# Kernel tuning notes

Measured on AMD Instinct MI355X. Metric: run time of the kernel, lower is better.

The kernel has to match this reference:

```python
import jax, jax.numpy as jnp
import numpy as np

IN_DIM = 128
OUT_DIM = 128
H = 8
HD = OUT_DIM // H  # 16
EPS = 1e-5
NEG = -1e30


def setup_inputs() -> dict:
    key = jax.random.key(0)
    ks = jax.random.split(key, 10)
    B, N = 8, 1024
    h = jax.random.normal(ks[0], (B, N, IN_DIM), dtype=jnp.float32)
    adj_mask = jax.random.randint(ks[1], (B, N, N), 0, 2, dtype=jnp.int32)
    s = 1.0 / np.sqrt(IN_DIM)
    W = jax.random.normal(ks[2], (H, IN_DIM, HD), dtype=jnp.float32) * s
    a = jax.random.normal(ks[3], (H, 2 * HD), dtype=jnp.float32) * (1.0 / np.sqrt(2 * HD))
    ln1_g = jnp.ones((OUT_DIM,), jnp.float32)
    ln1_b = jnp.zeros((OUT_DIM,), jnp.float32)
    w1 = jax.random.normal(ks[4], (OUT_DIM, 2 * OUT_DIM), dtype=jnp.float32) * (1.0 / np.sqrt(OUT_DIM))
    b1 = jnp.zeros((2 * OUT_DIM,), jnp.float32)
    w2 = jax.random.normal(ks[5], (2 * OUT_DIM, OUT_DIM), dtype=jnp.float32) * (1.0 / np.sqrt(2 * OUT_DIM))
    b2 = jnp.zeros((OUT_DIM,), jnp.float32)
    ln2_g = jnp.ones((OUT_DIM,), jnp.float32)
    ln2_b = jnp.zeros((OUT_DIM,), jnp.float32)
    return dict(h=h, adj_mask=adj_mask, W=W, a=a, ln1_g=ln1_g, ln1_b=ln1_b,
                w1=w1, b1=b1, w2=w2, b2=b2, ln2_g=ln2_g, ln2_b=ln2_b)


def _layernorm(x, g, b):
    mu = jnp.mean(x, axis=-1, keepdims=True)
    var = jnp.mean(jnp.square(x - mu), axis=-1, keepdims=True)
    return (x - mu) * jax.lax.rsqrt(var + EPS) * g + b


def reference(h, adj_mask, W, a, ln1_g, ln1_b, w1, b1, w2, b2, ln2_g, ln2_b):
    B, N, _ = h.shape
    # Per-head projection: (B,H,N,HD)
    Wh = jnp.einsum('bni,hid->bhnd', h, W)
    # a.[Wh_i, Wh_j] = a_src.Wh_i + a_dst.Wh_j (decompose concat-score)
    a_src, a_dst = a[:, :HD], a[:, HD:]
    s_i = jnp.einsum('bhnd,hd->bhn', Wh, a_src)  # source term
    s_j = jnp.einsum('bhnd,hd->bhn', Wh, a_dst)  # target term
    e = s_i[:, :, :, None] + s_j[:, :, None, :]  # (B,H,N,N)
    e = jnp.where(e >= 0, e, 0.2 * e)            # LeakyReLU(0.2)
    mask = (adj_mask != 0)[:, None, :, :]        # (B,1,N,N)
    e = jnp.where(mask, e, NEG)
    alpha = jax.nn.softmax(e, axis=-1)
    # rows with no neighbors -> NaN in torch softmax -> zeroed; replicate
    row_valid = jnp.any(mask, axis=-1, keepdims=True)  # (B,1,N,1)
    alpha = jnp.where(row_valid, alpha, 0.0)
    # dropout in eval mode = identity
    h_heads = jnp.einsum('bhnm,bhmd->bhnd', alpha, Wh)
    h_cat = h_heads.transpose(0, 2, 1, 3).reshape(B, N, H * HD)
    # residual (in_dim == out_dim here)
    h_cat = _layernorm(h_cat + h, ln1_g, ln1_b)
    ffn = jnp.maximum(h_cat @ w1 + b1, 0.0) @ w2 + b2
    return _layernorm(h_cat + ffn, ln2_g, ln2_b)
```

## Files before the change

kernel.cpp:

```cpp
#include <hip/hip_runtime.h>
#include <hip/hip_bf16.h>

#define IN_DIM 128
#define OUT_DIM 128
#define NHEAD 8
#define HD 16
#define BB 8
#define NN 1024
#define LOG2E 1.44269504f

typedef unsigned long long u64;
typedef float f32x4 __attribute__((ext_vector_type(4)));
typedef short bf16x8 __attribute__((ext_vector_type(8)));


__global__ __launch_bounds__(256) void k_prep(
    const float* __restrict__ hin, const float* __restrict__ W,
    const float* __restrict__ a, const int* __restrict__ adj,
    unsigned* __restrict__ bits_t, unsigned short* __restrict__ whT,
    float* __restrict__ si_g, float* __restrict__ sj_g,
    const float* __restrict__ w1, const float* __restrict__ w2,
    unsigned short* __restrict__ w1T, unsigned short* __restrict__ w2T)
{
    __shared__ float smem[32 * 132];
    int blk = blockIdx.x;
    int t = threadIdx.x;

    if (blk < 256) {
        int b = blk >> 5, ntile = blk & 31;
        const float* hrow = hin + ((size_t)b * NN + ntile * 32) * IN_DIM;
#pragma unroll
        for (int it = 0; it < 4; ++it) {
            int g = t + 256 * it;
            int row = g >> 5, c4 = g & 31;
            float4 v = ((const float4*)hrow)[g];
            *(float4*)&smem[row * 132 + c4 * 4] = v;
        }
        __syncthreads();

        int d4 = t & 3;
        int hq = (t >> 2) & 7;
        int ngrp = t >> 5;
        float acc[4][4];
#pragma unroll
        for (int q = 0; q < 4; ++q)
#pragma unroll
            for (int dd = 0; dd < 4; ++dd) acc[q][dd] = 0.f;

        for (int i4 = 0; i4 < 32; ++i4) {
            float4 wf[4];
#pragma unroll
            for (int k = 0; k < 4; ++k)
                wf[k] = *(const float4*)&W[((size_t)hq * 128 + i4 * 4 + k) * 16 + d4 * 4];
            float4 hv[4];
#pragma unroll
            for (int q = 0; q < 4; ++q)
                hv[q] = *(const float4*)&smem[(ngrp * 4 + q) * 132 + i4 * 4];
#pragma unroll
            for (int q = 0; q < 4; ++q) {
                acc[q][0] += hv[q].x * wf[0].x + hv[q].y * wf[1].x + hv[q].z * wf[2].x + hv[q].w * wf[3].x;
                acc[q][1] += hv[q].x * wf[0].y + hv[q].y * wf[1].y + hv[q].z * wf[2].y + hv[q].w * wf[3].y;
                acc[q][2] += hv[q].x * wf[0].z + hv[q].y * wf[1].z + hv[q].z * wf[2].z + hv[q].w * wf[3].z;
                acc[q][3] += hv[q].x * wf[0].w + hv[q].y * wf[1].w + hv[q].z * wf[2].w + hv[q].w * wf[3].w;
            }
        }

        int bh = b * NHEAD + hq;
        int rowbase = ntile * 32 + ngrp * 4;
        int p0 = ((rowbase >> 8) << 8) | ((rowbase >> 2) & 63);

        float asrc[4], adst[4];
#pragma unroll
        for (int dd = 0; dd < 4; ++dd) {
            asrc[dd] = a[hq * 32 + d4 * 4 + dd];
            adst[dd] = a[hq * 32 + 16 + d4 * 4 + dd];
        }
#pragma unroll
        for (int q = 0; q < 4; ++q) {
            float psi = acc[q][0] * asrc[0] + acc[q][1] * asrc[1] + acc[q][2] * asrc[2] + acc[q][3] * asrc[3];
            float psj = acc[q][0] * adst[0] + acc[q][1] * adst[1] + acc[q][2] * adst[2] + acc[q][3] * adst[3];
            psi += __shfl_xor(psi, 1); psi += __shfl_xor(psi, 2);
            psj += __shfl_xor(psj, 1); psj += __shfl_xor(psj, 2);
            if (d4 == 0) {
                si_g[(size_t)bh * NN + rowbase + q] = psi * LOG2E;
                sj_g[(size_t)bh * NN + p0 + q * 64] = psj * LOG2E;
            }
        }

#pragma unroll
        for (int dd = 0; dd < 4; ++dd) {
            unsigned u0, u1;
            asm("v_cvt_pk_bf16_f32 %0, %1, %2" : "=v"(u0) : "v"(acc[0][dd]), "v"(acc[1][dd]));
            asm("v_cvt_pk_bf16_f32 %0, %1, %2" : "=v"(u1) : "v"(acc[2][dd]), "v"(acc[3][dd]));
            size_t basei = (size_t)(bh * 16 + d4 * 4 + dd) * 1024 + p0;
            whT[basei]       = (unsigned short)(u0 & 0xffff);
            whT[basei + 64]  = (unsigned short)(u0 >> 16);
            whT[basei + 128] = (unsigned short)(u1 & 0xffff);
            whT[basei + 192] = (unsigned short)(u1 >> 16);
        }
    } else if (blk < 2304) {
        int lane = t & 63;
        int wave_id = (blk - 256) * 4 + (t >> 6);
        int b = wave_id >> 10, i = wave_id & 1023;
        const int4* rowp = (const int4*)(adj + ((size_t)(b * 1024 + i)) * 1024);
        int4 v0 = rowp[lane];
        int4 v1 = rowp[64 + lane];
        int4 v2 = rowp[128 + lane];
        int4 v3 = rowp[192 + lane];
        u64 B0x = __ballot(v0.x != 0), B0y = __ballot(v0.y != 0), B0z = __ballot(v0.z != 0), B0w = __ballot(v0.w != 0);
        u64 B1x = __ballot(v1.x != 0), B1y = __ballot(v1.y != 0), B1z = __ballot(v1.z != 0), B1w = __ballot(v1.w != 0);
        u64 B2x = __ballot(v2.x != 0), B2y = __ballot(v2.y != 0), B2z = __ballot(v2.z != 0), B2w = __ballot(v2.w != 0);
        u64 B3x = __ballot(v3.x != 0), B3y = __ballot(v3.y != 0), B3z = __ballot(v3.z != 0), B3w = __ballot(v3.w != 0);
        if (lane == 0) {
            unsigned* dst = bits_t + (size_t)b * 32 * 1024 + i;
#define STW(ch, c, B) \
            dst[((ch) * 8 + (c) * 2 + 0) * 1024] = (unsigned)(B); \
            dst[((ch) * 8 + (c) * 2 + 1) * 1024] = (unsigned)((B) >> 32);
            STW(0, 0, B0x) STW(0, 1, B0y) STW(0, 2, B0z) STW(0, 3, B0w)
            STW(1, 0, B1x) STW(1, 1, B1y) STW(1, 2, B1z) STW(1, 3, B1w)
            STW(2, 0, B2x) STW(2, 1, B2y) STW(2, 2, B2z) STW(2, 3, B2w)
            STW(3, 0, B3x) STW(3, 1, B3y) STW(3, 2, B3z) STW(3, 3, B3w)
#undef STW
        }
    } else {
        int bb = blk - 2304;
        const float* src; unsigned short* dst; int R, C;
        if (bb < 32) { src = w1; dst = w1T; R = 128; C = 256; }
        else         { src = w2; dst = w2T; R = 256; C = 128; bb -= 32; }
        int tpr = C >> 5;
        int tr = bb / tpr, tc = bb - tr * tpr;
        int r0 = tr << 5, c0 = tc << 5;
        int lr = t >> 5, lc = t & 31;
#pragma unroll
        for (int p = 0; p < 4; ++p)
            smem[(lr + p * 8) * 33 + lc] = src[(size_t)(r0 + lr + p * 8) * C + c0 + lc];
        __syncthreads();
#pragma unroll
        for (int p = 0; p < 4; ++p) {
            __hip_bfloat16 bv = __float2bfloat16(smem[lc * 33 + lr + p * 8]);
            dst[(size_t)(c0 + lr + p * 8) * R + r0 + lc] = *(unsigned short*)&bv;
        }
    }
}

__global__ __launch_bounds__(512, 3) void k_attn(
    const unsigned short* __restrict__ whT,
    const unsigned* __restrict__ bits_t,
    const float* __restrict__ si_g, const float* __restrict__ sj_g,
    float* __restrict__ hh)
{
    __shared__ __align__(16) unsigned short whT_s[16 * 1032];
    __shared__ __align__(16) float ejp_s[NN];
    __shared__ __align__(16) float ejn_s[NN];
    int t = threadIdx.x;
    int blk = blockIdx.x;
    int part = blk & 7;
    int bh = blk >> 3;
    int hq = bh & 7, b = bh >> 3;
    int blkrow = part * 128;

    {
        const uint4* src = (const uint4*)(whT + (size_t)bh * 16 * 1024);
#pragma unroll
        for (int it = 0; it < 4; ++it) {
            int g = t + 512 * it;
            int d = g >> 7, c8 = g & 127;
            uint4 v = src[g];
            *(uint4*)&whT_s[d * 1032 + c8 * 8] = v;
        }
#pragma unroll
        for (int jt = 0; jt < 2; ++jt) {
            int j = t + jt * 512;
            float sjv = sj_g[(size_t)bh * NN + j];
            float ep, en;
            asm("v_exp_f32 %0, %1" : "=v"(ep) : "v"(sjv));
            asm("v_exp_f32 %0, %1" : "=v"(en) : "v"(0.2f * sjv));
            ejp_s[j] = ep;
            ejn_s[j] = en;
        }
    }
    __syncthreads();

    int wv = t >> 6, lane = t & 63;
    int lo16 = lane & 15, g = lane >> 4;
    int row = blkrow + wv * 16 + lo16;
    float siL = si_g[(size_t)bh * NN + row];
    float esip, esin;
    asm("v_exp_f32 %0, %1" : "=v"(esip) : "v"(siL));
    asm("v_exp_f32 %0, %1" : "=v"(esin) : "v"(0.2f * siL));
    const unsigned* mcol = bits_t + (size_t)b * 32 * 1024 + row;

    f32x4 acc = {0.f, 0.f, 0.f, 0.f};
    float lsA = 0.f, lsB = 0.f;
    unsigned m = mcol[0];
#pragma unroll 4
    for (int kt = 0; kt < 32; ++kt) {
        unsigned m_next = (kt < 31) ? mcol[(size_t)(kt + 1) * 1024] : 0u;
        bf16x8 bfrag = *(const bf16x8*)&whT_s[lo16 * 1032 + kt * 32 + g * 8];
        float4 pa = *(const float4*)&ejp_s[kt * 32 + g * 8];
        float4 pb = *(const float4*)&ejp_s[kt * 32 + g * 8 + 4];
        float4 na = *(const float4*)&ejn_s[kt * 32 + g * 8];
        float4 nb = *(const float4*)&ejn_s[kt * 32 + g * 8 + 4];
        unsigned mm = m >> (g * 8);
        float ep[8] = {pa.x, pa.y, pa.z, pa.w, pb.x, pb.y, pb.z, pb.w};
        float en[8] = {na.x, na.y, na.z, na.w, nb.x, nb.y, nb.z, nb.w};
        union { bf16x8 v; unsigned u[4]; } af;
#pragma unroll
        for (int e2 = 0; e2 < 4; ++e2) {
            float q0 = fmaxf(esip * ep[2 * e2], esin * en[2 * e2]);
            float q1 = fmaxf(esip * ep[2 * e2 + 1], esin * en[2 * e2 + 1]);
            q0 = ((mm >> (2 * e2)) & 1) ? q0 : 0.f;
            q1 = ((mm >> (2 * e2 + 1)) & 1) ? q1 : 0.f;
            lsA += q0;
            lsB += q1;
            asm("v_cvt_pk_bf16_f32 %0, %1, %2" : "=v"(af.u[e2]) : "v"(q0), "v"(q1));
        }
        acc = __builtin_amdgcn_mfma_f32_16x16x32_bf16(af.v, bfrag, acc, 0, 0, 0);
        m = m_next;
    }

    float lsum = lsA + lsB;
    lsum += __shfl_xor(lsum, 16);
    lsum += __shfl_xor(lsum, 32);

    float* obase = hh + ((size_t)b * NN + blkrow + wv * 16) * OUT_DIM + hq * HD + lo16;
#pragma unroll
    for (int q = 0; q < 4; ++q) {
        float ls = __shfl(lsum, 4 * g + q);
        float r = (ls > 0.f) ? 1.0f / ls : 0.f;
        obase[(size_t)(4 * g + q) * OUT_DIM] = acc[q] * r;
    }
}

__global__ __launch_bounds__(512, 1) void k_ffn(const float* __restrict__ hhs,
                                                const float* __restrict__ hin,
                                                const float* __restrict__ g1,
                                                const float* __restrict__ bt1,
                                                const unsigned short* __restrict__ w1T,
                                                const float* __restrict__ bb1,
                                                const unsigned short* __restrict__ w2T,
                                                const float* __restrict__ bb2,
                                                const float* __restrict__ g2,
                                                const float* __restrict__ bt2,
                                                float* __restrict__ out) {
    __shared__ float xc_f[32][128];
    __shared__ float y_f[32][132];
    __shared__ __align__(16) unsigned short xc_bf[32 * 128];
    __shared__ __align__(16) unsigned short hid_bf[32 * 256];

    int t = threadIdx.x;
    int R0 = blockIdx.x * 32;
    int wv = t >> 6, lane = t & 63;
    int lo = lane & 15, g = lane >> 4;

    bf16x8 b1f[2][4];
#pragma unroll
    for (int jt = 0; jt < 2; ++jt) {
        int n = (wv * 2 + jt) * 16 + lo;
#pragma unroll
        for (int kt = 0; kt < 4; ++kt)
            b1f[jt][kt] = *(const bf16x8*)&w1T[(size_t)n * 128 + kt * 32 + g * 8];
    }
    bf16x8 b2f[8];
    {
        int n = wv * 16 + lo;
#pragma unroll
        for (int kt = 0; kt < 8; ++kt)
            b2f[kt] = *(const bf16x8*)&w2T[(size_t)n * 256 + kt * 32 + g * 8];
    }
    float b1v[2];
    b1v[0] = bb1[(wv * 2 + 0) * 16 + lo];
    b1v[1] = bb1[(wv * 2 + 1) * 16 + lo];
    float b2v = bb2[wv * 16 + lo];

    {
        int r = t >> 4, c = t & 15;
        size_t row = (size_t)(R0 + r) * 128;
        float4 ha = *(const float4*)&hhs[row + c * 8];
        float4 hb = *(const float4*)&hhs[row + c * 8 + 4];
        float4 ia = *(const float4*)&hin[row + c * 8];
        float4 ib = *(const float4*)&hin[row + c * 8 + 4];
        float x[8] = {ha.x + ia.x, ha.y + ia.y, ha.z + ia.z, ha.w + ia.w,
                      hb.x + ib.x, hb.y + ib.y, hb.z + ib.z, hb.w + ib.w};
        float s = 0.f, s2 = 0.f;
#pragma unroll
        for (int j = 0; j < 8; ++j) { s += x[j]; s2 += x[j] * x[j]; }
#pragma unroll
        for (int off = 8; off > 0; off >>= 1) {
            s += __shfl_xor(s, off);
            s2 += __shfl_xor(s2, off);
        }
        float mu = s * (1.f / 128.f);
        float var = s2 * (1.f / 128.f) - mu * mu;
        float rs = rsqrtf(var + 1e-5f);
        float4 ga = *(const float4*)&g1[c * 8], gb = *(const float4*)&g1[c * 8 + 4];
        float4 ba = *(const float4*)&bt1[c * 8], bb = *(const float4*)&bt1[c * 8 + 4];
        float gg[8] = {ga.x, ga.y, ga.z, ga.w, gb.x, gb.y, gb.z, gb.w};
        float bbv[8] = {ba.x, ba.y, ba.z, ba.w, bb.x, bb.y, bb.z, bb.w};
        float xo[8];
#pragma unroll
        for (int j = 0; j < 8; ++j) xo[j] = (x[j] - mu) * rs * gg[j] + bbv[j];
        *(float4*)&xc_f[r][c * 8]     = make_float4(xo[0], xo[1], xo[2], xo[3]);
        *(float4*)&xc_f[r][c * 8 + 4] = make_float4(xo[4], xo[5], xo[6], xo[7]);
        union { uint4 v; unsigned u[4]; } pk;
#pragma unroll
        for (int q = 0; q < 4; ++q)
            asm("v_cvt_pk_bf16_f32 %0, %1, %2" : "=v"(pk.u[q]) : "v"(xo[2 * q]), "v"(xo[2 * q + 1]));
        int byte = (r * 256 + c * 16) ^ ((r & 7) << 4);
        *(uint4*)((char*)xc_bf + byte) = pk.v;
    }
    __syncthreads();

    {
        bf16x8 af[2][4];
#pragma unroll
        for (int mt = 0; mt < 2; ++mt) {
            int m = mt * 16 + lo;
#pragma unroll
            for (int kt = 0; kt < 4; ++kt) {
                int byte = (m * 256 + kt * 64 + g * 16) ^ ((m & 7) << 4);
                af[mt][kt] = *(const bf16x8*)((const char*)xc_bf + byte);
            }
        }
#pragma unroll
        for (int mt = 0; mt < 2; ++mt)
#pragma unroll
            for (int jt = 0; jt < 2; ++jt) {
                f32x4 acc = {0.f, 0.f, 0.f, 0.f};
#pragma unroll
                for (int kt = 0; kt < 4; ++kt)
                    acc = __builtin_amdgcn_mfma_f32_16x16x32_bf16(af[mt][kt], b1f[jt][kt], acc, 0, 0, 0);
                int n = (wv * 2 + jt) * 16 + lo;
#pragma unroll
                for (int q = 0; q < 4; ++q) {
                    float hv = fmaxf(acc[q] + b1v[jt], 0.f);
                    int m = mt * 16 + 4 * g + q;
                    int byte = (m * 512 + n * 2) ^ ((m & 7) << 4);
                    __hip_bfloat16 bv = __float2bfloat16(hv);
                    *(unsigned short*)((char*)hid_bf + byte) = *(unsigned short*)&bv;
                }
            }
    }
    __syncthreads();

    {
        f32x4 acc2[2] = {{0.f, 0.f, 0.f, 0.f}, {0.f, 0.f, 0.f, 0.f}};
#pragma unroll
        for (int mt = 0; mt < 2; ++mt) {
            int m = mt * 16 + lo;
#pragma unroll
            for (int kt = 0; kt < 8; ++kt) {
                int byte = (m * 512 + kt * 64 + g * 16) ^ ((m & 7) << 4);
                bf16x8 a = *(const bf16x8*)((const char*)hid_bf + byte);
                acc2[mt] = __builtin_amdgcn_mfma_f32_16x16x32_bf16(a, b2f[kt], acc2[mt], 0, 0, 0);
            }
        }
        int n = wv * 16 + lo;
#pragma unroll
        for (int mt = 0; mt < 2; ++mt)
#pragma unroll
            for (int q = 0; q < 4; ++q)
                y_f[mt * 16 + 4 * g + q][n] = acc2[mt][q] + b2v;
    }
    __syncthreads();

    {
        int r = t >> 4, c = t & 15;
        float xv[8];
        float s = 0.f, s2 = 0.f;
#pragma unroll
        for (int j = 0; j < 8; ++j) {
            float v = xc_f[r][c * 8 + j] + y_f[r][c * 8 + j];
            xv[j] = v; s += v; s2 += v * v;
        }
#pragma unroll
        for (int off = 8; off > 0; off >>= 1) {
            s += __shfl_xor(s, off);
            s2 += __shfl_xor(s2, off);
        }
        float mu = s * (1.f / 128.f);
        float var = s2 * (1.f / 128.f) - mu * mu;
        float rs = rsqrtf(var + 1e-5f);
        float4 ga = *(const float4*)&g2[c * 8], gb = *(const float4*)&g2[c * 8 + 4];
        float4 ba = *(const float4*)&bt2[c * 8], bb = *(const float4*)&bt2[c * 8 + 4];
        float o[8] = {(xv[0] - mu) * rs * ga.x + ba.x, (xv[1] - mu) * rs * ga.y + ba.y,
                      (xv[2] - mu) * rs * ga.z + ba.z, (xv[3] - mu) * rs * ga.w + ba.w,
                      (xv[4] - mu) * rs * gb.x + bb.x, (xv[5] - mu) * rs * gb.y + bb.y,
                      (xv[6] - mu) * rs * gb.z + bb.z, (xv[7] - mu) * rs * gb.w + bb.w};
        size_t row = (size_t)(R0 + r) * 128;
        *(float4*)&out[row + c * 8]     = make_float4(o[0], o[1], o[2], o[3]);
        *(float4*)&out[row + c * 8 + 4] = make_float4(o[4], o[5], o[6], o[7]);
    }
}

extern "C" void kernel_launch(void* const* d_in, const int* in_sizes, int n_in,
                              void* d_out, int out_size, void* d_ws, size_t ws_size,
                              hipStream_t stream) {
    const float* hin  = (const float*)d_in[0];
    const int*   adj  = (const int*)d_in[1];
    const float* W    = (const float*)d_in[2];
    const float* a    = (const float*)d_in[3];
    const float* ln1g = (const float*)d_in[4];
    const float* ln1b = (const float*)d_in[5];
    const float* w1   = (const float*)d_in[6];
    const float* b1   = (const float*)d_in[7];
    const float* w2   = (const float*)d_in[8];
    const float* b2   = (const float*)d_in[9];
    const float* ln2g = (const float*)d_in[10];
    const float* ln2b = (const float*)d_in[11];
    float* out = (float*)d_out;

    unsigned* bits_t    = (unsigned*)d_ws;
    unsigned short* whT = (unsigned short*)((char*)d_ws + (1u << 20));
    float* si_g         = (float*)((char*)d_ws + (3u << 20));
    float* sj_g         = (float*)((char*)d_ws + (3u << 20) + (256u << 10));
    float* hh           = (float*)((char*)d_ws + (3u << 20) + (512u << 10));
    unsigned short* w1T = (unsigned short*)((char*)d_ws + (7u << 20) + (512u << 10));
    unsigned short* w2T = (unsigned short*)((char*)d_ws + (7u << 20) + (512u << 10) + 65536);

    k_prep<<<2368, 256, 0, stream>>>(hin, W, a, adj, bits_t, whT, si_g, sj_g,
                                     w1, w2, w1T, w2T);
    k_attn<<<BB * NHEAD * 8, 512, 0, stream>>>(whT, bits_t, si_g, sj_g, hh);
    k_ffn<<<BB * NN / 32, 512, 0, stream>>>(hh, hin, ln1g, ln1b, w1T, b1, w2T, b2, ln2g, ln2b, out);
}
```

Measured before the change: 64.20 us.

## Split prep kernel into separate launches and stage transposed W in LDS

```diff
diff --git a/kernel.cpp b/kernel.cpp
--- a/kernel.cpp
+++ b/kernel.cpp
@@ -14,132 +14,149 @@
 typedef short bf16x8 __attribute__((ext_vector_type(8)));
 
 
-__global__ __launch_bounds__(256) void k_prep(
+__global__ __launch_bounds__(256) void k_wh(
     const float* __restrict__ hin, const float* __restrict__ W,
-    const float* __restrict__ a, const int* __restrict__ adj,
-    unsigned* __restrict__ bits_t, unsigned short* __restrict__ whT,
-    float* __restrict__ si_g, float* __restrict__ sj_g,
-    const float* __restrict__ w1, const float* __restrict__ w2,
-    unsigned short* __restrict__ w1T, unsigned short* __restrict__ w2T)
+    const float* __restrict__ a,
+    unsigned short* __restrict__ whT, float* __restrict__ si_g,
+    float* __restrict__ sj_g)
 {
-    __shared__ float smem[32 * 132];
+    extern __shared__ float smem[];
+    float* h_s  = smem;
+    float* wt_s = smem + 32 * 132;
+    int t = threadIdx.x;
     int blk = blockIdx.x;
+    int b = blk >> 5;
+    int ntile = blk & 31;
+    const float* hrow = hin + ((size_t)b * NN + ntile * 32) * IN_DIM;
+
+#pragma unroll
+    for (int it = 0; it < 4; ++it) {
+        int g = t + 256 * it;
+        int row = g >> 5, c4 = g & 31;
+        float4 v = ((const float4*)hrow)[g];
+        *(float4*)&h_s[row * 132 + c4 * 4] = v;
+    }
+    for (int g = t; g < (NHEAD * IN_DIM * HD) / 4; g += 256) {
+        int hh = g >> 9;
+        int rem = g & 511;
+        int i = rem >> 2, d4 = rem & 3;
+        float4 v = ((const float4*)W)[g];
+        wt_s[(hh * 16 + d4 * 4 + 0) * 132 + i] = v.x;
+        wt_s[(hh * 16 + d4 * 4 + 1) * 132 + i] = v.y;
+        wt_s[(hh * 16 + d4 * 4 + 2) * 132 + i] = v.z;
+        wt_s[(hh * 16 + d4 * 4 + 3) * 132 + i] = v.w;
+    }
+    __syncthreads();
+
+    int d4 = t & 3;
+    int hq = (t >> 2) & 7;
+    int ngrp = t >> 5;
+    float acc[4][4];
+#pragma unroll
+    for (int q = 0; q < 4; ++q)
+#pragma unroll
+        for (int dd = 0; dd < 4; ++dd) acc[q][dd] = 0.f;
+
+    for (int i4 = 0; i4 < 32; ++i4) {
+        float4 wr[4], hv[4];
+#pragma unroll
+        for (int dd = 0; dd < 4; ++dd)
+            wr[dd] = *(const float4*)&wt_s[(hq * 16 + d4 * 4 + dd) * 132 + i4 * 4];
+#pragma unroll
+        for (int q = 0; q < 4; ++q)
+            hv[q] = *(const float4*)&h_s[(ngrp * 4 + q) * 132 + i4 * 4];
+#pragma unroll
+        for (int q = 0; q < 4; ++q)
+#pragma unroll
+            for (int dd = 0; dd < 4; ++dd)
+                acc[q][dd] += hv[q].x * wr[dd].x + hv[q].y * wr[dd].y +
+                              hv[q].z * wr[dd].z + hv[q].w * wr[dd].w;
+    }
+
+    int bh = b * NHEAD + hq;
+    int rowbase = ntile * 32 + ngrp * 4;
+    int p0 = ((rowbase >> 8) << 8) | ((rowbase >> 2) & 63);
+
+    float asrc[4], adst[4];
+#pragma unroll
+    for (int dd = 0; dd < 4; ++dd) {
+        asrc[dd] = a[hq * 32 + d4 * 4 + dd];
+        adst[dd] = a[hq * 32 + 16 + d4 * 4 + dd];
+    }
+#pragma unroll
+    for (int q = 0; q < 4; ++q) {
+        float psi = acc[q][0] * asrc[0] + acc[q][1] * asrc[1] + acc[q][2] * asrc[2] + acc[q][3] * asrc[3];
+        float psj = acc[q][0] * adst[0] + acc[q][1] * adst[1] + acc[q][2] * adst[2] + acc[q][3] * adst[3];
+        psi += __shfl_xor(psi, 1); psi += __shfl_xor(psi, 2);
+        psj += __shfl_xor(psj, 1); psj += __shfl_xor(psj, 2);
+        if (d4 == 0) {
+            si_g[(size_t)bh * NN + rowbase + q] = psi * LOG2E;
+            sj_g[(size_t)bh * NN + p0 + q * 64] = psj * LOG2E;
+        }
+    }
+
+#pragma unroll
+    for (int dd = 0; dd < 4; ++dd) {
+        unsigned u0, u1;
+        asm("v_cvt_pk_bf16_f32 %0, %1, %2" : "=v"(u0) : "v"(acc[0][dd]), "v"(acc[1][dd]));
+        asm("v_cvt_pk_bf16_f32 %0, %1, %2" : "=v"(u1) : "v"(acc[2][dd]), "v"(acc[3][dd]));
+        size_t basei = (size_t)(bh * 16 + d4 * 4 + dd) * 1024 + p0;
+        whT[basei]       = (unsigned short)(u0 & 0xffff);
+        whT[basei + 64]  = (unsigned short)(u0 >> 16);
+        whT[basei + 128] = (unsigned short)(u1 & 0xffff);
+        whT[basei + 192] = (unsigned short)(u1 >> 16);
+    }
+}
+
+__global__ __launch_bounds__(256) void k_pack(const int* __restrict__ adj,
+                                              unsigned* __restrict__ bits_t) {
     int t = threadIdx.x;
-
-    if (blk < 256) {
-        int b = blk >> 5, ntile = blk & 31;
-        const float* hrow = hin + ((size_t)b * NN + ntile * 32) * IN_DIM;
-#pragma unroll
-        for (int it = 0; it < 4; ++it) {
-            int g = t + 256 * it;
-            int row = g >> 5, c4 = g & 31;
-            float4 v = ((const float4*)hrow)[g];
-            *(float4*)&smem[row * 132 + c4 * 4] = v;
-        }
-        __syncthreads();
-
-        int d4 = t & 3;
-        int hq = (t >> 2) & 7;
-        int ngrp = t >> 5;
-        float acc[4][4];
-#pragma unroll
-        for (int q = 0; q < 4; ++q)
-#pragma unroll
-            for (int dd = 0; dd < 4; ++dd) acc[q][dd] = 0.f;
-
-        for (int i4 = 0; i4 < 32; ++i4) {
-            float4 wf[4];
-#pragma unroll
-            for (int k = 0; k < 4; ++k)
-                wf[k] = *(const float4*)&W[((size_t)hq * 128 + i4 * 4 + k) * 16 + d4 * 4];
-            float4 hv[4];
-#pragma unroll
-            for (int q = 0; q < 4; ++q)
-                hv[q] = *(const float4*)&smem[(ngrp * 4 + q) * 132 + i4 * 4];
-#pragma unroll
-            for (int q = 0; q < 4; ++q) {
-                acc[q][0] += hv[q].x * wf[0].x + hv[q].y * wf[1].x + hv[q].z * wf[2].x + hv[q].w * wf[3].x;
-                acc[q][1] += hv[q].x * wf[0].y + hv[q].y * wf[1].y + hv[q].z * wf[2].y + hv[q].w * wf[3].y;
-                acc[q][2] += hv[q].x * wf[0].z + hv[q].y * wf[1].z + hv[q].z * wf[2].z + hv[q].w * wf[3].z;
-                acc[q][3] += hv[q].x * wf[0].w + hv[q].y * wf[1].w + hv[q].z * wf[2].w + hv[q].w * wf[3].w;
-            }
-        }
-
-        int bh = b * NHEAD + hq;
-        int rowbase = ntile * 32 + ngrp * 4;
-        int p0 = ((rowbase >> 8) << 8) | ((rowbase >> 2) & 63);
-
-        float asrc[4], adst[4];
-#pragma unroll
-        for (int dd = 0; dd < 4; ++dd) {
-            asrc[dd] = a[hq * 32 + d4 * 4 + dd];
-            adst[dd] = a[hq * 32 + 16 + d4 * 4 + dd];
-        }
-#pragma unroll
-        for (int q = 0; q < 4; ++q) {
-            float psi = acc[q][0] * asrc[0] + acc[q][1] * asrc[1] + acc[q][2] * asrc[2] + acc[q][3] * asrc[3];
-            float psj = acc[q][0] * adst[0] + acc[q][1] * adst[1] + acc[q][2] * adst[2] + acc[q][3] * adst[3];
-            psi += __shfl_xor(psi, 1); psi += __shfl_xor(psi, 2);
-            psj += __shfl_xor(psj, 1); psj += __shfl_xor(psj, 2);
-            if (d4 == 0) {
-                si_g[(size_t)bh * NN + rowbase + q] = psi * LOG2E;
-                sj_g[(size_t)bh * NN + p0 + q * 64] = psj * LOG2E;
-            }
-        }
-
-#pragma unroll
-        for (int dd = 0; dd < 4; ++dd) {
-            unsigned u0, u1;
-            asm("v_cvt_pk_bf16_f32 %0, %1, %2" : "=v"(u0) : "v"(acc[0][dd]), "v"(acc[1][dd]));
-            asm("v_cvt_pk_bf16_f32 %0, %1, %2" : "=v"(u1) : "v"(acc[2][dd]), "v"(acc[3][dd]));
-            size_t basei = (size_t)(bh * 16 + d4 * 4 + dd) * 1024 + p0;
-            whT[basei]       = (unsigned short)(u0 & 0xffff);
-            whT[basei + 64]  = (unsigned short)(u0 >> 16);
-            whT[basei + 128] = (unsigned short)(u1 & 0xffff);
-            whT[basei + 192] = (unsigned short)(u1 >> 16);
-        }
-    } else if (blk < 2304) {
-        int lane = t & 63;
-        int wave_id = (blk - 256) * 4 + (t >> 6);
-        int b = wave_id >> 10, i = wave_id & 1023;
-        const int4* rowp = (const int4*)(adj + ((size_t)(b * 1024 + i)) * 1024);
-        int4 v0 = rowp[lane];
-        int4 v1 = rowp[64 + lane];
-        int4 v2 = rowp[128 + lane];
-        int4 v3 = rowp[192 + lane];
-        u64 B0x = __ballot(v0.x != 0), B0y = __ballot(v0.y != 0), B0z = __ballot(v0.z != 0), B0w = __ballot(v0.w != 0);
-        u64 B1x = __ballot(v1.x != 0), B1y = __ballot(v1.y != 0), B1z = __ballot(v1.z != 0), B1w = __ballot(v1.w != 0);
-        u64 B2x = __ballot(v2.x != 0), B2y = __ballot(v2.y != 0), B2z = __ballot(v2.z != 0), B2w = __ballot(v2.w != 0);
-        u64 B3x = __ballot(v3.x != 0), B3y = __ballot(v3.y != 0), B3z = __ballot(v3.z != 0), B3w = __ballot(v3.w != 0);
-        if (lane == 0) {
-            unsigned* dst = bits_t + (size_t)b * 32 * 1024 + i;
+    int lane = t & 63;
+    int wave_id = blockIdx.x * 4 + (t >> 6);
+    int b = wave_id >> 10, i = wave_id & 1023;
+    const int4* rowp = (const int4*)(adj + ((size_t)(b * 1024 + i)) * 1024);
+    int4 v0 = rowp[lane];
+    int4 v1 = rowp[64 + lane];
+    int4 v2 = rowp[128 + lane];
+    int4 v3 = rowp[192 + lane];
+    u64 B0x = __ballot(v0.x != 0), B0y = __ballot(v0.y != 0), B0z = __ballot(v0.z != 0), B0w = __ballot(v0.w != 0);
+    u64 B1x = __ballot(v1.x != 0), B1y = __ballot(v1.y != 0), B1z = __ballot(v1.z != 0), B1w = __ballot(v1.w != 0);
+    u64 B2x = __ballot(v2.x != 0), B2y = __ballot(v2.y != 0), B2z = __ballot(v2.z != 0), B2w = __ballot(v2.w != 0);
+    u64 B3x = __ballot(v3.x != 0), B3y = __ballot(v3.y != 0), B3z = __ballot(v3.z != 0), B3w = __ballot(v3.w != 0);
+    if (lane == 0) {
+        unsigned* dst = bits_t + (size_t)b * 32 * 1024 + i;
 #define STW(ch, c, B) \
-            dst[((ch) * 8 + (c) * 2 + 0) * 1024] = (unsigned)(B); \
-            dst[((ch) * 8 + (c) * 2 + 1) * 1024] = (unsigned)((B) >> 32);
-            STW(0, 0, B0x) STW(0, 1, B0y) STW(0, 2, B0z) STW(0, 3, B0w)
-            STW(1, 0, B1x) STW(1, 1, B1y) STW(1, 2, B1z) STW(1, 3, B1w)
-            STW(2, 0, B2x) STW(2, 1, B2y) STW(2, 2, B2z) STW(2, 3, B2w)
-            STW(3, 0, B3x) STW(3, 1, B3y) STW(3, 2, B3z) STW(3, 3, B3w)
+        dst[((ch) * 8 + (c) * 2 + 0) * 1024] = (unsigned)(B); \
+        dst[((ch) * 8 + (c) * 2 + 1) * 1024] = (unsigned)((B) >> 32);
+        STW(0, 0, B0x) STW(0, 1, B0y) STW(0, 2, B0z) STW(0, 3, B0w)
+        STW(1, 0, B1x) STW(1, 1, B1y) STW(1, 2, B1z) STW(1, 3, B1w)
+        STW(2, 0, B2x) STW(2, 1, B2y) STW(2, 2, B2z) STW(2, 3, B2w)
+        STW(3, 0, B3x) STW(3, 1, B3y) STW(3, 2, B3z) STW(3, 3, B3w)
 #undef STW
-        }
-    } else {
-        int bb = blk - 2304;
-        const float* src; unsigned short* dst; int R, C;
-        if (bb < 32) { src = w1; dst = w1T; R = 128; C = 256; }
-        else         { src = w2; dst = w2T; R = 256; C = 128; bb -= 32; }
-        int tpr = C >> 5;
-        int tr = bb / tpr, tc = bb - tr * tpr;
-        int r0 = tr << 5, c0 = tc << 5;
-        int lr = t >> 5, lc = t & 31;
-#pragma unroll
-        for (int p = 0; p < 4; ++p)
-            smem[(lr + p * 8) * 33 + lc] = src[(size_t)(r0 + lr + p * 8) * C + c0 + lc];
-        __syncthreads();
-#pragma unroll
-        for (int p = 0; p < 4; ++p) {
-            __hip_bfloat16 bv = __float2bfloat16(smem[lc * 33 + lr + p * 8]);
-            dst[(size_t)(c0 + lr + p * 8) * R + r0 + lc] = *(unsigned short*)&bv;
-        }
+    }
+}
+
+__global__ __launch_bounds__(256) void k_wprep(const float* __restrict__ w1,
+                                               const float* __restrict__ w2,
+                                               unsigned short* __restrict__ w1T,
+                                               unsigned short* __restrict__ w2T) {
+    __shared__ float tile[32][33];
+    int blk = blockIdx.x;
+    const float* src; unsigned short* dst; int R, C;
+    if (blk < 32) { src = w1; dst = w1T; R = 128; C = 256; }
+    else          { src = w2; dst = w2T; R = 256; C = 128; blk -= 32; }
+    int tpr = C >> 5;
+    int tr = blk / tpr, tc = blk - tr * tpr;
+    int r0 = tr << 5, c0 = tc << 5;
+    int t = threadIdx.x, lr = t >> 5, lc = t & 31;
+#pragma unroll
+    for (int p = 0; p < 4; ++p)
+        tile[lr + p * 8][lc] = src[(size_t)(r0 + lr + p * 8) * C + c0 + lc];
+    __syncthreads();
+#pragma unroll
+    for (int p = 0; p < 4; ++p) {
+        __hip_bfloat16 bv = __float2bfloat16(tile[lc][lr + p * 8]);
+        dst[(size_t)(c0 + lr + p * 8) * R + r0 + lc] = *(unsigned short*)&bv;
     }
 }
 
@@ -418,8 +435,9 @@
     unsigned short* w1T = (unsigned short*)((char*)d_ws + (7u << 20) + (512u << 10));
     unsigned short* w2T = (unsigned short*)((char*)d_ws + (7u << 20) + (512u << 10) + 65536);
 
-    k_prep<<<2368, 256, 0, stream>>>(hin, W, a, adj, bits_t, whT, si_g, sj_g,
-                                     w1, w2, w1T, w2T);
+    k_pack<<<2048, 256, 0, stream>>>(adj, bits_t);
+    k_wh<<<BB * 32, 256, (32 * 132 + 128 * 132) * sizeof(float), stream>>>(hin, W, a, whT, si_g, sj_g);
+    k_wprep<<<64, 256, 0, stream>>>(w1, w2, w1T, w2T);
     k_attn<<<BB * NHEAD * 8, 512, 0, stream>>>(whT, bits_t, si_g, sj_g, hh);
     k_ffn<<<BB * NN / 32, 512, 0, stream>>>(hh, hin, ln1g, ln1b, w1T, b1, w2T, b2, ln2g, ln2b, out);
 }
```

Result: faster. 59.17 us (-7.8%).
